# Optimization experiments

Measured on AMD Instinct MI355X. Metric: run time of the kernel, lower is better.

## Reference

```python
import jax, jax.numpy as jnp
import numpy as np

N_NODES = 100000
N_EDGES = 2000000
N_GRAPHS = 1024
HIDDEN = 32
LATENT = 8


def setup_inputs() -> dict:
    key = jax.random.key(0)
    ks = jax.random.split(key, 12)
    x = jax.random.normal(ks[0], (N_NODES, 1), dtype=jnp.float32)
    edge_index = jax.random.randint(ks[1], (2, N_EDGES), 0, N_NODES, dtype=jnp.int32)
    batch = jnp.sort(jax.random.randint(ks[2], (N_NODES,), 0, N_GRAPHS, dtype=jnp.int32))
    s = 0.1
    W = jax.random.normal(ks[3], (1, HIDDEN), dtype=jnp.float32) * s
    b = jax.random.normal(ks[4], (HIDDEN,), dtype=jnp.float32) * s
    w_mu = jax.random.normal(ks[5], (HIDDEN, LATENT), dtype=jnp.float32) * s
    b_mu = jax.random.normal(ks[6], (LATENT,), dtype=jnp.float32) * s
    w_lv = jax.random.normal(ks[7], (HIDDEN, LATENT), dtype=jnp.float32) * s
    b_lv = jax.random.normal(ks[8], (LATENT,), dtype=jnp.float32) * s
    w_dec = jax.random.normal(ks[9], (LATENT, 100), dtype=jnp.float32) * s
    b_dec = jax.random.normal(ks[10], (100,), dtype=jnp.float32) * s
    eps = jax.random.normal(ks[11], (N_GRAPHS, LATENT), dtype=jnp.float32)
    return {"x": x, "edge_index": edge_index, "batch": batch, "W": W, "b": b,
            "w_mu": w_mu, "b_mu": b_mu, "w_lv": w_lv, "b_lv": b_lv,
            "w_dec": w_dec, "b_dec": b_dec, "eps": eps}


def gcn_conv(x, edge_index, W, b):
    # PyG GCNConv: add self-loops, symmetric D^-1/2 (A+I) D^-1/2 normalization
    n = x.shape[0]
    loop = jnp.arange(n, dtype=edge_index.dtype)
    src = jnp.concatenate([edge_index[0], loop])
    dst = jnp.concatenate([edge_index[1], loop])
    deg = jax.ops.segment_sum(jnp.ones_like(dst, dtype=x.dtype), dst, num_segments=n)
    dinv = jnp.where(deg > 0, jax.lax.rsqrt(jnp.maximum(deg, 1.0)), 0.0)
    norm = dinv[src] * dinv[dst]          # [E+N]
    h = x @ W                              # [N, hidden] (tiny GEMM)
    msg = h[src] * norm[:, None]           # gather + scale (memory bound)
    out = jax.ops.segment_sum(msg, dst, num_segments=n)  # scatter-add
    return out + b


def reference(x, edge_index, batch, W, b, w_mu, b_mu, w_lv, b_lv, w_dec, b_dec, eps):
    G = eps.shape[0]
    h = jax.nn.relu(gcn_conv(x, edge_index, W, b))       # [N, hidden]
    sums = jax.ops.segment_sum(h, batch, num_segments=G)
    cnts = jax.ops.segment_sum(jnp.ones((h.shape[0],), h.dtype), batch, num_segments=G)
    pooled = sums / jnp.maximum(cnts, 1.0)[:, None]      # global_mean_pool [G, hidden]
    mu = pooled @ w_mu + b_mu                            # [G, latent]
    logvar = pooled @ w_lv + b_lv
    z = mu + eps * jnp.exp(0.5 * logvar)                 # reparam
    adj_logits = (z @ w_dec + b_dec).reshape(-1, 10, 10)
    adj = (jax.nn.sigmoid(adj_logits) > 0.5).astype(jnp.float32)
    return adj, mu, logvar
```

## Files before the change

### kernel.cpp

```cpp
#include <hip/hip_runtime.h>

#define HID 32
#define LAT 8
#define BSH 8
#define BUCK 256
#define CAPSH 13
#define CB 512
#define PB 512
#define PEV 16
#define PCHUNK (PB * PEV)

__device__ __forceinline__ double atomAddF64(double* p, double v) {
    return unsafeAtomicAdd(p, v);
}

__global__ void zero_kernel(unsigned* __restrict__ p, int n) {
    int i = blockIdx.x * blockDim.x + threadIdx.x;
    if (i < n) p[i] = 0;
}


__global__ __launch_bounds__(PB)
void place3_kernel(const unsigned* __restrict__ src, const unsigned* __restrict__ dst,
                   int E, int HBn,
                   unsigned* __restrict__ cursor, unsigned* __restrict__ csr) {
    __shared__ unsigned cnt[512];
    __shared__ unsigned gbase[512];
    uint4 dv[PEV / 4];
    uint4 sv[PEV / 4];
    unsigned rank[PEV];
    int tid = threadIdx.x;

    cnt[tid] = 0;
    __syncthreads();

    int E4 = E >> 2;
    int base4 = blockIdx.x * (PCHUNK / 4);
    #pragma unroll
    for (int k = 0; k < PEV / 4; k++) {
        int i4 = base4 + k * PB + tid;
        if (i4 < E4) {
            dv[k] = ((const uint4*)dst)[i4];
            sv[k] = ((const uint4*)src)[i4];
            rank[4 * k + 0] = atomicAdd(&cnt[dv[k].x >> BSH], 1u);
            rank[4 * k + 1] = atomicAdd(&cnt[dv[k].y >> BSH], 1u);
            rank[4 * k + 2] = atomicAdd(&cnt[dv[k].z >> BSH], 1u);
            rank[4 * k + 3] = atomicAdd(&cnt[dv[k].w >> BSH], 1u);
        }
    }
    __syncthreads();

    for (int j = tid; j < HBn; j += PB) {
        unsigned c = cnt[j];
        gbase[j] = c ? atomicAdd(&cursor[j], c) : 0u;
    }
    __syncthreads();

    #pragma unroll
    for (int k = 0; k < PEV / 4; k++) {
        int i4 = base4 + k * PB + tid;
        if (i4 < E4) {
            unsigned d, s, bin, r;
            d = dv[k].x; s = sv[k].x; bin = d >> BSH; r = gbase[bin] + rank[4 * k + 0];
            if (r < (1u << CAPSH)) csr[((size_t)bin << CAPSH) + r] = ((d & (BUCK - 1u)) << 17) | s;
            d = dv[k].y; s = sv[k].y; bin = d >> BSH; r = gbase[bin] + rank[4 * k + 1];
            if (r < (1u << CAPSH)) csr[((size_t)bin << CAPSH) + r] = ((d & (BUCK - 1u)) << 17) | s;
            d = dv[k].z; s = sv[k].z; bin = d >> BSH; r = gbase[bin] + rank[4 * k + 2];
            if (r < (1u << CAPSH)) csr[((size_t)bin << CAPSH) + r] = ((d & (BUCK - 1u)) << 17) | s;
            d = dv[k].w; s = sv[k].w; bin = d >> BSH; r = gbase[bin] + rank[4 * k + 3];
            if (r < (1u << CAPSH)) csr[((size_t)bin << CAPSH) + r] = ((d & (BUCK - 1u)) << 17) | s;
        }
    }
}

__global__ __launch_bounds__(CB)
void bdeg_kernel(const unsigned* __restrict__ cursor, const unsigned* __restrict__ csr,
                 int N, int G,
                 const float* __restrict__ x, const int* __restrict__ batch,
                 float* __restrict__ dinv, float* __restrict__ y32,
                 int* __restrict__ startArr) {
    int b = blockIdx.x;
    __shared__ unsigned cnt[BUCK];
    if (threadIdx.x < BUCK) cnt[threadIdx.x] = 0;
    __syncthreads();
    unsigned n = min(cursor[b], (unsigned)(1u << CAPSH));
    const unsigned* seg = csr + ((size_t)b << CAPSH);
    unsigned n4 = n >> 2;
    for (unsigned i = threadIdx.x; i < n4; i += CB) {
        uint4 v = ((const uint4*)seg)[i];
        atomicAdd(&cnt[v.x >> 17], 1u);
        atomicAdd(&cnt[v.y >> 17], 1u);
        atomicAdd(&cnt[v.z >> 17], 1u);
        atomicAdd(&cnt[v.w >> 17], 1u);
    }
    unsigned t = (n4 << 2) + threadIdx.x;
    if (t < n) atomicAdd(&cnt[seg[t] >> 17], 1u);
    __syncthreads();
    if (threadIdx.x < BUCK) {
        int node = (b << BSH) + threadIdx.x;
        if (node < N) {
            double dv = 1.0 / sqrt((double)(cnt[threadIdx.x] + 1));
            dinv[node] = (float)dv;
            y32[node] = (float)((double)x[node] * dv);
            int b1 = batch[node];
            if (node == 0) { for (int g = 0; g <= b1; g++) startArr[g] = 0; }
            else { int bp = batch[node - 1]; for (int g = bp + 1; g <= b1; g++) startArr[g] = node; }
            if (node == N - 1) { for (int g = b1 + 1; g <= G; g++) startArr[g] = N; }
        }
    }
}

__global__ __launch_bounds__(CB)
void bsum_kernel(const unsigned* __restrict__ cursor, const unsigned* __restrict__ csr,
                 int N,
                 const float* __restrict__ dinv, const float* __restrict__ y32,
                 double* __restrict__ acc) {
    int b = blockIdx.x;
    __shared__ double accs[BUCK];
    if (threadIdx.x < BUCK) accs[threadIdx.x] = 0.0;
    __syncthreads();
    unsigned n = min(cursor[b], (unsigned)(1u << CAPSH));
    const unsigned* seg = csr + ((size_t)b << CAPSH);
    unsigned n4 = n >> 2;
    for (unsigned i = threadIdx.x; i < n4; i += CB) {
        uint4 v = ((const uint4*)seg)[i];
        float ya = y32[v.x & 0x1FFFFu];
        float yb = y32[v.y & 0x1FFFFu];
        float yc = y32[v.z & 0x1FFFFu];
        float yd = y32[v.w & 0x1FFFFu];
        atomicAdd(&accs[v.x >> 17], (double)ya);
        atomicAdd(&accs[v.y >> 17], (double)yb);
        atomicAdd(&accs[v.z >> 17], (double)yc);
        atomicAdd(&accs[v.w >> 17], (double)yd);
    }
    unsigned t = (n4 << 2) + threadIdx.x;
    if (t < n) {
        unsigned v = seg[t];
        atomicAdd(&accs[v >> 17], (double)y32[v & 0x1FFFFu]);
    }
    __syncthreads();
    if (threadIdx.x < BUCK) {
        int node = (b << BSH) + threadIdx.x;
        if (node < N)
            acc[node] = (double)dinv[node] * ((double)y32[node] + accs[threadIdx.x]);
    }
}


__global__ void deg_kernel(const int* __restrict__ dst, int E, int* __restrict__ deg) {
    int e = blockIdx.x * blockDim.x + threadIdx.x;
    if (e < E) atomicAdd(&deg[dst[e]], 1);
}
__global__ void y_kernel(const float* __restrict__ x, const int* __restrict__ deg,
                         int N, double* __restrict__ y, double* __restrict__ acc) {
    int i = blockIdx.x * blockDim.x + threadIdx.x;
    if (i < N) {
        double dv = 1.0 / sqrt((double)(deg[i] + 1));
        double yi = (double)x[i] * dv;
        y[i] = yi; acc[i] = yi;
    }
}
__global__ void scatter_kernel(const int* __restrict__ ei, int E,
                               const double* __restrict__ y, double* __restrict__ acc) {
    int e = blockIdx.x * blockDim.x + threadIdx.x;
    if (e < E) atomAddF64(&acc[ei[E + e]], y[ei[e]]);
}
__global__ void finalize_kernel(const int* __restrict__ deg, int N, double* __restrict__ acc) {
    int i = blockIdx.x * blockDim.x + threadIdx.x;
    if (i < N) acc[i] *= 1.0 / sqrt((double)(deg[i] + 1));
}
__global__ void bounds_kernel(const int* __restrict__ batch, int N, int G,
                              int* __restrict__ start) {
    int i = blockIdx.x * blockDim.x + threadIdx.x;
    if (i >= N) return;
    int b1 = batch[i];
    if (i == 0) { for (int g = 0; g <= b1; g++) start[g] = 0; }
    else { int b0 = batch[i - 1]; for (int g = b0 + 1; g <= b1; g++) start[g] = i; }
    if (i == N - 1) { for (int g = b1 + 1; g <= G; g++) start[g] = N; }
}


__global__ __launch_bounds__(64)
void graph_kernel(const int* __restrict__ start, const double* __restrict__ acc,
                  const float* __restrict__ W, const float* __restrict__ b,
                  const float* __restrict__ w_mu, const float* __restrict__ b_mu,
                  const float* __restrict__ w_lv, const float* __restrict__ b_lv,
                  const float* __restrict__ w_dec, const float* __restrict__ b_dec,
                  const float* __restrict__ eps,
                  float* __restrict__ out, int G) {
    int g = blockIdx.x, lane = threadIdx.x;
    int s0 = start[g], s1 = start[g + 1];

    double hacc[HID];
    #pragma unroll
    for (int j = 0; j < HID; j++) hacc[j] = 0.0;

    for (int i = s0 + lane; i < s1; i += 64) {
        double s = acc[i];
        #pragma unroll
        for (int j = 0; j < HID; j++) {
            double h = (double)W[j] * s + (double)b[j];
            hacc[j] += (h > 0.0) ? h : 0.0;
        }
    }

    #pragma unroll
    for (int m = 1; m < 64; m <<= 1) {
        #pragma unroll
        for (int j = 0; j < HID; j++) hacc[j] += __shfl_xor(hacc[j], m, 64);
    }

    int c = s1 - s0;
    double denom = (c > 0) ? (double)c : 1.0;
    #pragma unroll
    for (int j = 0; j < HID; j++) hacc[j] /= denom;

    double mv = 0.0;
    if (lane < 16) {
        int l = lane & (LAT - 1);
        const float* wm = (lane < LAT) ? w_mu : w_lv;
        const float* bm = (lane < LAT) ? b_mu : b_lv;
        double a = (double)bm[l];
        #pragma unroll
        for (int j = 0; j < HID; j++) a += hacc[j] * (double)wm[j * LAT + l];
        mv = a;
        if (lane < LAT) out[(size_t)G * 100 + (size_t)g * LAT + l] = (float)a;
        else            out[(size_t)G * 100 + (size_t)G * LAT + (size_t)g * LAT + l] = (float)a;
    }

    double z[LAT];
    #pragma unroll
    for (int l = 0; l < LAT; l++) {
        double mu_l = __shfl(mv, l, 64);
        double lv_l = __shfl(mv, l + LAT, 64);
        z[l] = mu_l + (double)eps[(size_t)g * LAT + l] * exp(0.5 * lv_l);
    }

    for (int t = lane; t < 100; t += 64) {
        double lg = (double)b_dec[t];
        #pragma unroll
        for (int l = 0; l < LAT; l++) lg += z[l] * (double)w_dec[l * 100 + t];
        out[(size_t)g * 100 + t] = (lg > 0.0) ? 1.0f : 0.0f;
    }
}

extern "C" void kernel_launch(void* const* d_in, const int* in_sizes, int n_in,
                              void* d_out, int out_size, void* d_ws, size_t ws_size,
                              hipStream_t stream) {
    const float* x     = (const float*)d_in[0];
    const int*   ei    = (const int*)d_in[1];
    const int*   batch = (const int*)d_in[2];
    const float* W     = (const float*)d_in[3];
    const float* b     = (const float*)d_in[4];
    const float* w_mu  = (const float*)d_in[5];
    const float* b_mu  = (const float*)d_in[6];
    const float* w_lv  = (const float*)d_in[7];
    const float* b_lv  = (const float*)d_in[8];
    const float* w_dec = (const float*)d_in[9];
    const float* b_dec = (const float*)d_in[10];
    const float* eps   = (const float*)d_in[11];

    int N = in_sizes[0];
    int E = in_sizes[1] / 2;
    int G = in_sizes[11] / LAT;
    float* out = (float*)d_out;

    int HBn = (N + BUCK - 1) >> BSH;
    int NBp = (E + PCHUNK - 1) / PCHUNK;

    char* ws = (char*)d_ws;
    const int bs = 256;

    size_t off = 0;
    double*   acc    = (double*)(ws + off);   off += (size_t)N * 8;
    unsigned* csr    = (unsigned*)(ws + off); off += ((size_t)HBn << CAPSH) * 4;
    unsigned* cursor = (unsigned*)(ws + off); off += (size_t)HBn * 4;
    float*    dinv   = (float*)(ws + off);    off += (size_t)N * 4;
    float*    y32    = (float*)(ws + off);    off += (size_t)N * 4;
    int*      start  = (int*)(ws + off);      off += (size_t)(G + 1) * 4;
    size_t need = off;

    bool fast = (N <= 131072) && (HBn <= 512) && (ws_size >= need)
                && (E % 4 == 0)
                && ((long)E / HBn * 3 / 2 < (1L << CAPSH));

    if (fast) {
        zero_kernel<<<(HBn + bs - 1) / bs, bs, 0, stream>>>(cursor, HBn);
        place3_kernel<<<NBp, PB, 0, stream>>>((const unsigned*)ei, (const unsigned*)(ei + E),
                                              E, HBn, cursor, csr);
        bdeg_kernel<<<HBn, CB, 0, stream>>>(cursor, csr, N, G, x, batch, dinv, y32, start);
        bsum_kernel<<<HBn, CB, 0, stream>>>(cursor, csr, N, dinv, y32, acc);
    } else {
        size_t foff = 0;
        double* facc = (double*)(ws + foff); foff += (size_t)N * 8;
        double* fy   = (double*)(ws + foff); foff += (size_t)N * 8;
        int*    fdeg = (int*)(ws + foff);    foff += (size_t)N * 4;
        int*    fst  = (int*)(ws + foff);    foff += (size_t)(G + 1) * 4;
        acc = facc; start = fst;
        zero_kernel<<<(N + bs - 1) / bs, bs, 0, stream>>>((unsigned*)fdeg, N);
        deg_kernel<<<(E + bs - 1) / bs, bs, 0, stream>>>(ei + E, E, fdeg);
        y_kernel<<<(N + bs - 1) / bs, bs, 0, stream>>>(x, fdeg, N, fy, facc);
        scatter_kernel<<<(E + bs - 1) / bs, bs, 0, stream>>>(ei, E, fy, facc);
        finalize_kernel<<<(N + bs - 1) / bs, bs, 0, stream>>>(fdeg, N, facc);
        bounds_kernel<<<(N + bs - 1) / bs, bs, 0, stream>>>(batch, N, G, start);
    }

    graph_kernel<<<G, 64, 0, stream>>>(start, acc, W, b, w_mu, b_mu,
                                       w_lv, b_lv, w_dec, b_dec, eps, out, G);
}
```

Measured before the change: 52.11 us.

## Split bucket placement into count and scatter kernels to cut register pressure

The single placement kernel, which held 16 destination ids, 16 source ids and 16 ranks in registers across a block barrier, becomes two kernels. The first counts per-bucket edges in shared memory and reserves global offsets, storing them in a per-block matrix. The second reloads the edges, recomputes ranks with shared atomics and scatters packed entries into the CSR buckets. This frees registers to raise occupancy, but it costs a second read of the destination array, an extra launch, and a small global offset matrix.

New measurement: 55.08 us. 1.06x slower.

```diff
diff --git a/kernel.cpp b/kernel.cpp
--- a/kernel.cpp
+++ b/kernel.cpp
@@ -21,16 +21,10 @@
 
 
 __global__ __launch_bounds__(PB)
-void place3_kernel(const unsigned* __restrict__ src, const unsigned* __restrict__ dst,
-                   int E, int HBn,
-                   unsigned* __restrict__ cursor, unsigned* __restrict__ csr) {
+void placeA_kernel(const unsigned* __restrict__ dst, int E, int HBn,
+                   unsigned* __restrict__ cursor, unsigned* __restrict__ gmat) {
     __shared__ unsigned cnt[512];
-    __shared__ unsigned gbase[512];
-    uint4 dv[PEV / 4];
-    uint4 sv[PEV / 4];
-    unsigned rank[PEV];
     int tid = threadIdx.x;
-
     cnt[tid] = 0;
     __syncthreads();
 
@@ -40,34 +34,50 @@
     for (int k = 0; k < PEV / 4; k++) {
         int i4 = base4 + k * PB + tid;
         if (i4 < E4) {
-            dv[k] = ((const uint4*)dst)[i4];
-            sv[k] = ((const uint4*)src)[i4];
-            rank[4 * k + 0] = atomicAdd(&cnt[dv[k].x >> BSH], 1u);
-            rank[4 * k + 1] = atomicAdd(&cnt[dv[k].y >> BSH], 1u);
-            rank[4 * k + 2] = atomicAdd(&cnt[dv[k].z >> BSH], 1u);
-            rank[4 * k + 3] = atomicAdd(&cnt[dv[k].w >> BSH], 1u);
+            uint4 d = ((const uint4*)dst)[i4];
+            atomicAdd(&cnt[d.x >> BSH], 1u);
+            atomicAdd(&cnt[d.y >> BSH], 1u);
+            atomicAdd(&cnt[d.z >> BSH], 1u);
+            atomicAdd(&cnt[d.w >> BSH], 1u);
         }
     }
     __syncthreads();
 
+    unsigned* grow = gmat + (size_t)blockIdx.x * HBn;
     for (int j = tid; j < HBn; j += PB) {
         unsigned c = cnt[j];
-        gbase[j] = c ? atomicAdd(&cursor[j], c) : 0u;
-    }
-    __syncthreads();
-
+        grow[j] = c ? atomicAdd(&cursor[j], c) : 0u;
+    }
+}
+
+__global__ __launch_bounds__(PB)
+void placeB_kernel(const unsigned* __restrict__ src, const unsigned* __restrict__ dst,
+                   int E, int HBn,
+                   const unsigned* __restrict__ gmat, unsigned* __restrict__ csr) {
+    __shared__ unsigned cnt[512];
+    __shared__ unsigned gbase[512];
+    int tid = threadIdx.x;
+    cnt[tid] = 0;
+    const unsigned* grow = gmat + (size_t)blockIdx.x * HBn;
+    for (int j = tid; j < HBn; j += PB) gbase[j] = grow[j];
+    __syncthreads();
+
+    int E4 = E >> 2;
+    int base4 = blockIdx.x * (PCHUNK / 4);
     #pragma unroll
     for (int k = 0; k < PEV / 4; k++) {
         int i4 = base4 + k * PB + tid;
         if (i4 < E4) {
+            uint4 dv = ((const uint4*)dst)[i4];
+            uint4 sv = ((const uint4*)src)[i4];
             unsigned d, s, bin, r;
-            d = dv[k].x; s = sv[k].x; bin = d >> BSH; r = gbase[bin] + rank[4 * k + 0];
+            d = dv.x; s = sv.x; bin = d >> BSH; r = gbase[bin] + atomicAdd(&cnt[bin], 1u);
             if (r < (1u << CAPSH)) csr[((size_t)bin << CAPSH) + r] = ((d & (BUCK - 1u)) << 17) | s;
-            d = dv[k].y; s = sv[k].y; bin = d >> BSH; r = gbase[bin] + rank[4 * k + 1];
+            d = dv.y; s = sv.y; bin = d >> BSH; r = gbase[bin] + atomicAdd(&cnt[bin], 1u);
             if (r < (1u << CAPSH)) csr[((size_t)bin << CAPSH) + r] = ((d & (BUCK - 1u)) << 17) | s;
-            d = dv[k].z; s = sv[k].z; bin = d >> BSH; r = gbase[bin] + rank[4 * k + 2];
+            d = dv.z; s = sv.z; bin = d >> BSH; r = gbase[bin] + atomicAdd(&cnt[bin], 1u);
             if (r < (1u << CAPSH)) csr[((size_t)bin << CAPSH) + r] = ((d & (BUCK - 1u)) << 17) | s;
-            d = dv[k].w; s = sv[k].w; bin = d >> BSH; r = gbase[bin] + rank[4 * k + 3];
+            d = dv.w; s = sv.w; bin = d >> BSH; r = gbase[bin] + atomicAdd(&cnt[bin], 1u);
             if (r < (1u << CAPSH)) csr[((size_t)bin << CAPSH) + r] = ((d & (BUCK - 1u)) << 17) | s;
         }
     }
@@ -275,6 +285,7 @@
     double*   acc    = (double*)(ws + off);   off += (size_t)N * 8;
     unsigned* csr    = (unsigned*)(ws + off); off += ((size_t)HBn << CAPSH) * 4;
     unsigned* cursor = (unsigned*)(ws + off); off += (size_t)HBn * 4;
+    unsigned* gmat   = (unsigned*)(ws + off); off += (size_t)NBp * HBn * 4;
     float*    dinv   = (float*)(ws + off);    off += (size_t)N * 4;
     float*    y32    = (float*)(ws + off);    off += (size_t)N * 4;
     int*      start  = (int*)(ws + off);      off += (size_t)(G + 1) * 4;
@@ -286,8 +297,9 @@
 
     if (fast) {
         zero_kernel<<<(HBn + bs - 1) / bs, bs, 0, stream>>>(cursor, HBn);
-        place3_kernel<<<NBp, PB, 0, stream>>>((const unsigned*)ei, (const unsigned*)(ei + E),
-                                              E, HBn, cursor, csr);
+        placeA_kernel<<<NBp, PB, 0, stream>>>((const unsigned*)(ei + E), E, HBn, cursor, gmat);
+        placeB_kernel<<<NBp, PB, 0, stream>>>((const unsigned*)ei, (const unsigned*)(ei + E),
+                                              E, HBn, gmat, csr);
         bdeg_kernel<<<HBn, CB, 0, stream>>>(cursor, csr, N, G, x, batch, dinv, y32, start);
         bsum_kernel<<<HBn, CB, 0, stream>>>(cursor, csr, N, dinv, y32, acc);
     } else {
```
